# Kernel optimization log

Hardware: AMD Instinct MI355X
Metric: run time of the kernel (lower is better)

The kernel has to match this reference:

```python
import jax, jax.numpy as jnp
import numpy as np

DIM = 384; HEADS = 12; WS = 7; SHIFT = 3
IMG_H = 56; IMG_W = 56; B = 32; MLP_HID = 1536
N = WS * WS; HEAD_DIM = DIM // HEADS


def _rel_pos_index():
    # standard Swin relative position index, shape [N, N], values in [0, (2*WS-1)^2)
    coords = np.stack(np.meshgrid(np.arange(WS), np.arange(WS), indexing='ij')).reshape(2, -1)
    rel = (coords[:, :, None] - coords[:, None, :]).transpose(1, 2, 0)
    rel[..., 0] += WS - 1
    rel[..., 1] += WS - 1
    rel[..., 0] *= 2 * WS - 1
    return jnp.asarray(rel.sum(-1))

REL_IDX = _rel_pos_index()


def _shift_mask():
    # Swin shifted-window attention mask: 0 within region, -100 across regions
    img = np.zeros((IMG_H, IMG_W))
    cnt = 0
    for hs in (slice(0, -WS), slice(-WS, -SHIFT), slice(-SHIFT, None)):
        for ws_ in (slice(0, -WS), slice(-WS, -SHIFT), slice(-SHIFT, None)):
            img[hs, ws_] = cnt
            cnt += 1
    mw = img.reshape(IMG_H // WS, WS, IMG_W // WS, WS).transpose(0, 2, 1, 3).reshape(-1, N)
    am = mw[:, None, :] - mw[:, :, None]
    return jnp.asarray(np.where(am != 0, -100.0, 0.0).astype(np.float32))


def setup_inputs() -> dict:
    key = jax.random.key(0)
    ks = jax.random.split(key, 8)
    rn = lambda k, s: jax.random.normal(k, s, jnp.float32) * 0.02
    return {
        'x': jax.random.normal(ks[0], (B, IMG_H * IMG_W, DIM), jnp.float32),
        'mask': _shift_mask(),
        'w_ln1': jnp.ones((DIM,), jnp.float32), 'b_ln1': jnp.zeros((DIM,), jnp.float32),
        'w_qkv': rn(ks[1], (3 * DIM, DIM)), 'b_qkv': jnp.zeros((3 * DIM,), jnp.float32),
        'rel_bias': rn(ks[2], ((2 * WS - 1) ** 2, HEADS)),
        'w_proj': rn(ks[3], (DIM, DIM)), 'b_proj': jnp.zeros((DIM,), jnp.float32),
        'w_ln2': jnp.ones((DIM,), jnp.float32), 'b_ln2': jnp.zeros((DIM,), jnp.float32),
        'w_fc1': rn(ks[4], (MLP_HID, DIM)), 'b_fc1': jnp.zeros((MLP_HID,), jnp.float32),
        'w_fc2': rn(ks[5], (DIM, MLP_HID)), 'b_fc2': jnp.zeros((DIM,), jnp.float32),
        'H': IMG_H, 'W': IMG_W,
    }


def _ln(x, g, b, eps=1e-5):
    mu = x.mean(-1, keepdims=True)
    var = ((x - mu) ** 2).mean(-1, keepdims=True)
    return (x - mu) * jax.lax.rsqrt(var + eps) * g + b


def reference(x, mask, w_ln1, b_ln1, w_qkv, b_qkv, rel_bias, w_proj, b_proj,
              w_ln2, b_ln2, w_fc1, b_fc1, w_fc2, b_fc2, H, W):
    Bsz, L, C = x.shape
    nW = (H // WS) * (W // WS)
    shortcut = x
    h = _ln(x, w_ln1, b_ln1).reshape(Bsz, H, W, C)
    # cyclic shift
    h = jnp.roll(h, (-SHIFT, -SHIFT), axis=(1, 2))
    # window partition -> [B*nW, N, C]
    h = h.reshape(Bsz, H // WS, WS, W // WS, WS, C).transpose(0, 1, 3, 2, 4, 5).reshape(-1, N, C)
    nB = h.shape[0]
    qkv = (h @ w_qkv.T + b_qkv).reshape(nB, N, 3, HEADS, HEAD_DIM).transpose(2, 0, 3, 1, 4)
    q, k, v = qkv[0] * (HEAD_DIM ** -0.5), qkv[1], qkv[2]  # each [nB, heads, N, hd]
    attn = jnp.einsum('bhnd,bhmd->bhnm', q, k)
    bias = rel_bias[REL_IDX].transpose(2, 0, 1)  # [heads, N, N]
    attn = attn + bias[None]
    attn = attn.reshape(Bsz, nW, HEADS, N, N) + mask[None, :, None]
    attn = jax.nn.softmax(attn, axis=-1).reshape(nB, HEADS, N, N)
    o = jnp.einsum('bhnm,bhmd->bhnd', attn, v).transpose(0, 2, 1, 3).reshape(nB, N, C)
    o = o @ w_proj.T + b_proj
    # window reverse
    o = o.reshape(Bsz, H // WS, W // WS, WS, WS, C).transpose(0, 1, 3, 2, 4, 5).reshape(Bsz, H, W, C)
    o = jnp.roll(o, (SHIFT, SHIFT), axis=(1, 2)).reshape(Bsz, H * W, C)
    x = shortcut + o
    h2 = _ln(x, w_ln2, b_ln2)
    h2 = jax.nn.gelu(h2 @ w_fc1.T + b_fc1) @ w_fc2.T + b_fc2
    return x + h2
```

## Files before the change

### kernel.cpp

```cpp
#include <hip/hip_runtime.h>
#include <stdint.h>

#define B_     32
#define IMG    56
#define L_     (IMG*IMG)
#define C_     384
#define HEADS_ 12
#define HD     32
#define WS_    7
#define N_     49
#define NWIN   64
#define NB     (B_*NWIN)
#define M_TOK  (NB*N_)
#define QKVF   1152

typedef __attribute__((ext_vector_type(8))) short bf16x8;
typedef __attribute__((ext_vector_type(4))) float f32x4;
typedef __attribute__((ext_vector_type(4))) unsigned short u16x4;

__device__ __forceinline__ float bf2f(unsigned short u) {
  union { unsigned int u; float f; } c; c.u = ((unsigned int)u) << 16; return c.f;
}
__device__ __forceinline__ unsigned short f2bf(float f) {
  union { float f; unsigned int u; } c; c.f = f;
  unsigned int r = c.u + 0x7FFFu + ((c.u >> 16) & 1u);
  return (unsigned short)(r >> 16);
}

__device__ __forceinline__ void gload_lds16(const void* g, void* l) {
  __builtin_amdgcn_global_load_lds(
      (const __attribute__((address_space(1))) unsigned int*)(uintptr_t)g,
      (__attribute__((address_space(3))) unsigned int*)(uintptr_t)l,
      16, 0, 0);
}

#define MFMA16(a, b, c) __builtin_amdgcn_mfma_f32_16x16x32_bf16((a), (b), (c), 0, 0, 0)

__global__ __launch_bounds__(256) void k_f2b(const float* __restrict__ src,
                                             ushort* __restrict__ dst, int n) {
  int i = blockIdx.x * 256 + threadIdx.x;
  if (i < n) dst[i] = f2bf(src[i]);
}

template<bool WINDOW>
__global__ __launch_bounds__(256) void k_ln(const float* __restrict__ X,
    const float* __restrict__ G, const float* __restrict__ Bb,
    ushort* __restrict__ out)
{
  int token = blockIdx.x * 4 + (threadIdx.x >> 6);
  int lane  = threadIdx.x & 63;
  const float* xp = X + (size_t)token * C_;
  float v[6];
#pragma unroll
  for (int t = 0; t < 6; t++) v[t] = xp[lane + 64*t];
  float s = 0.f, s2 = 0.f;
#pragma unroll
  for (int t = 0; t < 6; t++) { s += v[t]; s2 += v[t]*v[t]; }
#pragma unroll
  for (int off = 32; off > 0; off >>= 1) {
    s  += __shfl_down(s,  off, 64);
    s2 += __shfl_down(s2, off, 64);
  }
  s = __shfl(s, 0, 64); s2 = __shfl(s2, 0, 64);
  float mu   = s * (1.f / C_);
  float rstd = rsqrtf(s2 * (1.f / C_) - mu * mu + 1e-5f);
  size_t obase;
  if (WINDOW) {
    int b = token / L_, pix = token % L_;
    int hi = pix / IMG, wj = pix % IMG;
    int sh = hi - 3; if (sh < 0) sh += IMG;
    int sw = wj - 3; if (sw < 0) sw += IMG;
    int w = b * NWIN + (sh / WS_) * 8 + (sw / WS_);
    int p = (sh % WS_) * WS_ + (sw % WS_);
    obase = ((size_t)w * N_ + p) * C_;
  } else {
    obase = (size_t)token * C_;
  }
#pragma unroll
  for (int t = 0; t < 6; t++) {
    int c = lane + 64*t;
    out[obase + c] = f2bf((v[t] - mu) * rstd * G[c] + Bb[c]);
  }
}

template<int EPI, typename OutT>
__global__ __launch_bounds__(256, 2) void k_gemm(
    const ushort* __restrict__ A, const ushort* __restrict__ W,
    const float* __restrict__ bias, OutT* __restrict__ out,
    const float* __restrict__ res, int M, int N, int K)
{
  __shared__ __align__(16) ushort As[2][128*32];
  __shared__ __align__(16) ushort Bs[2][128*32];
  int ntn = N >> 7;
  int nwg = gridDim.x;
  int bid = (blockIdx.x & 7) * (nwg >> 3) + (blockIdx.x >> 3);
  int m0 = (bid / ntn) << 7;
  int n0 = (bid % ntn) << 7;
  int tid  = threadIdx.x;
  int wave = tid >> 6, lane = tid & 63;
  int l15  = lane & 15, quad = lane >> 4;
  int wm = (wave & 1) << 6, wn = (wave >> 1) << 6;

  int srow0 = wave * 32 + (lane >> 2);
  int srow1 = srow0 + 16;
  int scol  = (lane & 3) * 8;
  const ushort* gA0 = A + (size_t)(m0 + srow0) * K + scol;
  const ushort* gA1 = A + (size_t)(m0 + srow1) * K + scol;
  const ushort* gB0 = W + (size_t)(n0 + srow0) * K + scol;
  const ushort* gB1 = W + (size_t)(n0 + srow1) * K + scol;
  int oA0 = srow0 * 32 + scol;
  int oA1 = srow1 * 32 + scol;

  f32x4 acc[4][4];
#pragma unroll
  for (int i = 0; i < 4; i++)
#pragma unroll
    for (int j = 0; j < 4; j++) acc[i][j] = (f32x4){0.f, 0.f, 0.f, 0.f};

  gload_lds16(gA0, &As[0][oA0]);
  gload_lds16(gA1, &As[0][oA1]);
  gload_lds16(gB0, &Bs[0][oA0]);
  gload_lds16(gB1, &Bs[0][oA1]);
  gA0 += 32; gA1 += 32; gB0 += 32; gB1 += 32;
  asm volatile("s_waitcnt vmcnt(0)" : : : "memory");
  __syncthreads();

  int nt = K >> 5;
  int cur = 0;
  for (int t = 0; t < nt; t++) {
    int nxt = cur ^ 1;
    if (t + 1 < nt) {
      gload_lds16(gA0, &As[nxt][oA0]);
      gload_lds16(gA1, &As[nxt][oA1]);
      gload_lds16(gB0, &Bs[nxt][oA0]);
      gload_lds16(gB1, &Bs[nxt][oA1]);
      gA0 += 32; gA1 += 32; gB0 += 32; gB1 += 32;
    }
    bf16x8 af[4], bfr[4];
#pragma unroll
    for (int i = 0; i < 4; i++) af[i]  = *(const bf16x8*)&As[cur][(wm + i*16 + l15)*32 + quad*8];
#pragma unroll
    for (int j = 0; j < 4; j++) bfr[j] = *(const bf16x8*)&Bs[cur][(wn + j*16 + l15)*32 + quad*8];
#pragma unroll
    for (int i = 0; i < 4; i++)
#pragma unroll
      for (int j = 0; j < 4; j++)
        acc[i][j] = MFMA16(af[i], bfr[j], acc[i][j]);
    asm volatile("s_waitcnt vmcnt(0)" : : : "memory");
    __syncthreads();
    cur = nxt;
  }

  float bv[4];
#pragma unroll
  for (int j = 0; j < 4; j++) bv[j] = bias[n0 + wn + j*16 + l15];
#pragma unroll
  for (int i = 0; i < 4; i++) {
#pragma unroll
    for (int r = 0; r < 4; r++) {
      int row = m0 + wm + i*16 + quad*4 + r;
      size_t dstbase;
      if (EPI == 1) {
        int w = row / N_, p = row % N_;
        int b = w >> 6, wi = w & 63;
        int hi = (wi >> 3) * WS_ + p / WS_ + 3; if (hi >= IMG) hi -= IMG;
        int wj = (wi & 7)  * WS_ + p % WS_ + 3; if (wj >= IMG) wj -= IMG;
        dstbase = ((size_t)b * L_ + hi * IMG + wj) * C_;
      } else {
        dstbase = (size_t)row * N;
      }
#pragma unroll
      for (int j = 0; j < 4; j++) {
        int col = n0 + wn + j*16 + l15;
        float v = acc[i][j][r] + bv[j];
        if (EPI == 2) {
          v = v / (1.f + __expf(-1.5957691216057308f * (v + 0.044715f * v * v * v)));
        }
        size_t dst = dstbase + col;
        if (EPI == 1) v += res[dst];
        if (EPI == 3) v += res[(size_t)row * N + col];
        if constexpr (sizeof(OutT) == 4) out[dst] = v;
        else                             out[dst] = f2bf(v);
      }
    }
  }
}

__global__ __launch_bounds__(256) void k_bm(const float* __restrict__ relb,
    const float* __restrict__ mask, ushort* __restrict__ bm)
{
  int n = blockIdx.x * 256 + threadIdx.x;
  int r    = n & 3;
  int col  = (n >> 2) & 63;
  int quad = (n >> 8) & 3;
  int i    = (n >> 10) & 3;
  int hw   = n >> 12;
  int h = hw % HEADS_, wc = hw / HEADS_;
  int row = i * 16 + quad * 4 + r;
  float v;
  if (col >= N_) v = -30000.f;
  else if (row >= N_) v = 0.f;
  else {
    int idx = (row / WS_ - col / WS_ + 6) * 13 + (row % WS_ - col % WS_ + 6);
    v = relb[idx * HEADS_ + h] + mask[((size_t)wc * N_ + row) * N_ + col];
  }
  bm[n] = f2bf(v);
}

__global__ __launch_bounds__(256, 3) void k_attn_mfma(
    const ushort* __restrict__ qkv, const ushort* __restrict__ bm,
    ushort* __restrict__ out)
{
  __shared__ __align__(16) ushort Ps[4][64*64];
  __shared__ __align__(16) ushort Vt[4][32*64];
  int wave = threadIdx.x >> 6, lane = threadIdx.x & 63;
  int task = blockIdx.x * 4 + wave;
  int w = task / HEADS_, h = task % HEADS_;
  int l15 = lane & 15, quad = lane >> 4;

  const ushort* base = qkv + (size_t)w * N_ * QKVF + h * HD;

  bf16x8 qf[4], kf[4];
#pragma unroll
  for (int i = 0; i < 4; i++) {
    int rr = i * 16 + l15; if (rr > 48) rr = 48;
    const ushort* rp = base + (size_t)rr * QKVF + quad * 8;
    qf[i] = *(const bf16x8*)rp;
    kf[i] = *(const bf16x8*)(rp + C_);
  }

  {
    int m = lane > 48 ? 48 : lane;
    const ushort* vp = base + (size_t)m * QKVF + 2 * C_;
    bf16x8 v0 = *(const bf16x8*)vp;
    bf16x8 v1 = *(const bf16x8*)(vp + 8);
    bf16x8 v2 = *(const bf16x8*)(vp + 16);
    bf16x8 v3 = *(const bf16x8*)(vp + 24);
    ushort* vt = &Vt[wave][0];
#pragma unroll
    for (int d = 0; d < 32; d++) {
      ushort val = (ushort)(d < 8 ? v0[d & 7] : d < 16 ? v1[d & 7]
                                  : d < 24 ? v2[d & 7] : v3[d & 7]);
      vt[d * 64 + (lane ^ ((d & 7) << 3))] = val;
    }
  }

  f32x4 acc[4][4];
#pragma unroll
  for (int i = 0; i < 4; i++)
#pragma unroll
    for (int j = 0; j < 4; j++) acc[i][j] = (f32x4){0.f, 0.f, 0.f, 0.f};
#pragma unroll
  for (int i = 0; i < 4; i++)
#pragma unroll
    for (int j = 0; j < 4; j++)
      acc[i][j] = MFMA16(qf[i], kf[j], acc[i][j]);

  const ushort* bmb = bm + ((size_t)(w & 63) * HEADS_ + h) * 4096;
  float sv[4][4][4];
#pragma unroll
  for (int i = 0; i < 4; i++)
#pragma unroll
    for (int j = 0; j < 4; j++) {
      u16x4 bv = *(const u16x4*)(bmb + (((i * 4 + quad) * 64) + (j * 16 + l15)) * 4);
#pragma unroll
      for (int r = 0; r < 4; r++)
        sv[i][j][r] = acc[i][j][r] * 0.17677669529663687f + bf2f(bv[r]);
    }

  float mx[4][4], sm[4][4];
#pragma unroll
  for (int i = 0; i < 4; i++)
#pragma unroll
    for (int r = 0; r < 4; r++)
      mx[i][r] = fmaxf(fmaxf(sv[i][0][r], sv[i][1][r]),
                       fmaxf(sv[i][2][r], sv[i][3][r]));
#pragma unroll
  for (int off = 1; off <= 8; off <<= 1)
#pragma unroll
    for (int i = 0; i < 4; i++)
#pragma unroll
      for (int r = 0; r < 4; r++)
        mx[i][r] = fmaxf(mx[i][r], __shfl_xor(mx[i][r], off, 64));
#pragma unroll
  for (int i = 0; i < 4; i++)
#pragma unroll
    for (int r = 0; r < 4; r++) sm[i][r] = 0.f;
#pragma unroll
  for (int i = 0; i < 4; i++)
#pragma unroll
    for (int j = 0; j < 4; j++)
#pragma unroll
      for (int r = 0; r < 4; r++) {
        float e = __expf(sv[i][j][r] - mx[i][r]);
        sv[i][j][r] = e;
        sm[i][r] += e;
      }
#pragma unroll
  for (int off = 1; off <= 8; off <<= 1)
#pragma unroll
    for (int i = 0; i < 4; i++)
#pragma unroll
      for (int r = 0; r < 4; r++)
        sm[i][r] += __shfl_xor(sm[i][r], off, 64);

  ushort* pw = &Ps[wave][0];
#pragma unroll
  for (int i = 0; i < 4; i++)
#pragma unroll
    for (int r = 0; r < 4; r++) {
      float inv = 1.f / sm[i][r];
      int row = i * 16 + quad * 4 + r;
      int s = (row & 7) << 3;
#pragma unroll
      for (int j = 0; j < 4; j++)
        pw[row * 64 + ((j * 16 + l15) ^ s)] = f2bf(sv[i][j][r] * inv);
    }

  f32x4 o[4][2];
#pragma unroll
  for (int i = 0; i < 4; i++)
#pragma unroll
    for (int jv = 0; jv < 2; jv++) o[i][jv] = (f32x4){0.f, 0.f, 0.f, 0.f};
  const ushort* vt = &Vt[wave][0];
#pragma unroll
  for (int ks = 0; ks < 2; ks++) {
    int kc = ks * 32 + quad * 8;
    bf16x8 pa[4], vb[2];
#pragma unroll
    for (int i = 0; i < 4; i++) {
      int row = i * 16 + l15;
      pa[i] = *(const bf16x8*)&pw[row * 64 + (kc ^ ((row & 7) << 3))];
    }
#pragma unroll
    for (int jv = 0; jv < 2; jv++) {
      int nn = jv * 16 + l15;
      vb[jv] = *(const bf16x8*)&vt[nn * 64 + (kc ^ ((nn & 7) << 3))];
    }
#pragma unroll
    for (int i = 0; i < 4; i++)
#pragma unroll
      for (int jv = 0; jv < 2; jv++)
        o[i][jv] = MFMA16(pa[i], vb[jv], o[i][jv]);
  }

  ushort* op = out + ((size_t)w * N_) * C_ + h * HD;
#pragma unroll
  for (int i = 0; i < 4; i++)
#pragma unroll
    for (int r = 0; r < 4; r++) {
      int row = i * 16 + quad * 4 + r;
      if (row < N_) {
#pragma unroll
        for (int jv = 0; jv < 2; jv++)
          op[(size_t)row * C_ + jv * 16 + l15] = f2bf(o[i][jv][r]);
      }
    }
}

extern "C" void kernel_launch(void* const* d_in, const int* in_sizes, int n_in,
                              void* d_out, int out_size, void* d_ws, size_t ws_size,
                              hipStream_t stream) {
  (void)in_sizes; (void)n_in; (void)out_size; (void)ws_size;
  const float* x      = (const float*)d_in[0];
  const float* mask   = (const float*)d_in[1];
  const float* w_ln1  = (const float*)d_in[2];
  const float* b_ln1  = (const float*)d_in[3];
  const float* w_qkv  = (const float*)d_in[4];
  const float* b_qkv  = (const float*)d_in[5];
  const float* relb   = (const float*)d_in[6];
  const float* w_proj = (const float*)d_in[7];
  const float* b_proj = (const float*)d_in[8];
  const float* w_ln2  = (const float*)d_in[9];
  const float* b_ln2  = (const float*)d_in[10];
  const float* w_fc1  = (const float*)d_in[11];
  const float* b_fc1  = (const float*)d_in[12];
  const float* w_fc2  = (const float*)d_in[13];
  const float* b_fc2  = (const float*)d_in[14];

  char* ws = (char*)d_ws;
  ushort* r0 = (ushort*)ws;
  ushort* r1 = (ushort*)(ws + 308281344);
  ushort* bmt = (ushort*)(ws + 231211008);
  ushort* wbq = (ushort*)(ws + 385351680);
  ushort* wbp = wbq + QKVF * C_;
  ushort* wb1 = wbp + C_ * C_;
  ushort* wb2 = wb1 + 1536 * C_;
  float*  x1   = (float*)d_out;
  float*  outp = (float*)d_out;

  k_f2b<<<(QKVF*C_ + 255)/256, 256, 0, stream>>>(w_qkv,  wbq, QKVF*C_);
  k_f2b<<<(C_*C_   + 255)/256, 256, 0, stream>>>(w_proj, wbp, C_*C_);
  k_f2b<<<(1536*C_ + 255)/256, 256, 0, stream>>>(w_fc1,  wb1, 1536*C_);
  k_f2b<<<(C_*1536 + 255)/256, 256, 0, stream>>>(w_fc2,  wb2, C_*1536);
  k_bm<<<(NWIN*HEADS_*4096)/256, 256, 0, stream>>>(relb, mask, bmt);

  k_ln<true ><<<M_TOK/4, 256, 0, stream>>>(x, w_ln1, b_ln1, r1);
  k_gemm<0, ushort><<<(M_TOK/128)*(QKVF/128), 256, 0, stream>>>(
      r1, wbq, b_qkv, r0, nullptr, M_TOK, QKVF, 384);
  k_attn_mfma<<<NB*HEADS_/4, 256, 0, stream>>>(r0, bmt, r1);
  k_gemm<1, float><<<(M_TOK/128)*(C_/128), 256, 0, stream>>>(
      r1, wbp, b_proj, x1, x, M_TOK, C_, 384);
  k_ln<false><<<M_TOK/4, 256, 0, stream>>>(x1, w_ln2, b_ln2, r1);
  k_gemm<2, ushort><<<(M_TOK/128)*(1536/128), 256, 0, stream>>>(
      r1, wb1, b_fc1, r0, nullptr, M_TOK, 1536, 384);
  k_gemm<3, float><<<(M_TOK/128)*(C_/128), 256, 0, stream>>>(
      r0, wb2, b_fc2, outp, x1, M_TOK, C_, 1536);
}
```

Baseline: 1.056 ms.

## Triple-buffer GEMM LDS tiles and XOR-swizzle layout to cut bank conflicts

The GEMM K-loop moves from double to triple buffering of the A and B tiles. Two tiles are prefetched ahead, and the loop waits with vmcnt(4) so the previous stage's global-to-LDS loads can stay in flight, using a single barrier per iteration. The LDS tile layout is also XOR-swizzled: the global source row and chunk are permuted at load time and the fragment reads apply a matching XOR. This is meant to reduce LDS bank conflicts on the 16-byte fragment reads. The cost is 50% more shared memory per block, which may affect the two-blocks-per-CU occupancy target, and more index arithmetic.

```diff
diff --git a/kernel.cpp b/kernel.cpp
--- a/kernel.cpp
+++ b/kernel.cpp
@@ -89,8 +89,8 @@
     const float* __restrict__ bias, OutT* __restrict__ out,
     const float* __restrict__ res, int M, int N, int K)
 {
-  __shared__ __align__(16) ushort As[2][128*32];
-  __shared__ __align__(16) ushort Bs[2][128*32];
+  __shared__ __align__(16) ushort As[3][128*32];
+  __shared__ __align__(16) ushort Bs[3][128*32];
   int ntn = N >> 7;
   int nwg = gridDim.x;
   int bid = (blockIdx.x & 7) * (nwg >> 3) + (blockIdx.x >> 3);
@@ -101,15 +101,17 @@
   int l15  = lane & 15, quad = lane >> 4;
   int wm = (wave & 1) << 6, wn = (wave >> 1) << 6;
 
-  int srow0 = wave * 32 + (lane >> 2);
-  int srow1 = srow0 + 16;
-  int scol  = (lane & 3) * 8;
-  const ushort* gA0 = A + (size_t)(m0 + srow0) * K + scol;
-  const ushort* gA1 = A + (size_t)(m0 + srow1) * K + scol;
-  const ushort* gB0 = W + (size_t)(n0 + srow0) * K + scol;
-  const ushort* gB1 = W + (size_t)(n0 + srow1) * K + scol;
-  int oA0 = srow0 * 32 + scol;
-  int oA1 = srow1 * 32 + scol;
+  int l2 = lane & 3;
+  int R0 = wave * 32 + (lane >> 2);
+  int R1 = R0 + 16;
+  int r0 = R0 ^ ((R0 >> 2) & 1), q0 = l2 ^ (r0 & 3);
+  int r1 = R1 ^ ((R1 >> 2) & 1), q1 = l2 ^ (r1 & 3);
+  const ushort* gA0 = A + (size_t)(m0 + r0) * K + q0 * 8;
+  const ushort* gA1 = A + (size_t)(m0 + r1) * K + q1 * 8;
+  const ushort* gB0 = W + (size_t)(n0 + r0) * K + q0 * 8;
+  const ushort* gB1 = W + (size_t)(n0 + r1) * K + q1 * 8;
+  int o0 = R0 * 32 + l2 * 8;
+  int o1 = R1 * 32 + l2 * 8;
 
   f32x4 acc[4][4];
 #pragma unroll
@@ -117,38 +119,49 @@
 #pragma unroll
     for (int j = 0; j < 4; j++) acc[i][j] = (f32x4){0.f, 0.f, 0.f, 0.f};
 
-  gload_lds16(gA0, &As[0][oA0]);
-  gload_lds16(gA1, &As[0][oA1]);
-  gload_lds16(gB0, &Bs[0][oA0]);
-  gload_lds16(gB1, &Bs[0][oA1]);
+  gload_lds16(gA0, &As[0][o0]);
+  gload_lds16(gA1, &As[0][o1]);
+  gload_lds16(gB0, &Bs[0][o0]);
+  gload_lds16(gB1, &Bs[0][o1]);
   gA0 += 32; gA1 += 32; gB0 += 32; gB1 += 32;
-  asm volatile("s_waitcnt vmcnt(0)" : : : "memory");
-  __syncthreads();
+  gload_lds16(gA0, &As[1][o0]);
+  gload_lds16(gA1, &As[1][o1]);
+  gload_lds16(gB0, &Bs[1][o0]);
+  gload_lds16(gB1, &Bs[1][o1]);
+  gA0 += 32; gA1 += 32; gB0 += 32; gB1 += 32;
 
   int nt = K >> 5;
-  int cur = 0;
+  int cur = 0, stg = 2;
   for (int t = 0; t < nt; t++) {
-    int nxt = cur ^ 1;
-    if (t + 1 < nt) {
-      gload_lds16(gA0, &As[nxt][oA0]);
-      gload_lds16(gA1, &As[nxt][oA1]);
-      gload_lds16(gB0, &Bs[nxt][oA0]);
-      gload_lds16(gB1, &Bs[nxt][oA1]);
+    if (t + 1 < nt) asm volatile("s_waitcnt vmcnt(4)" ::: "memory");
+    else            asm volatile("s_waitcnt vmcnt(0)" ::: "memory");
+    __builtin_amdgcn_s_barrier();
+    asm volatile("" ::: "memory");
+    if (t + 2 < nt) {
+      gload_lds16(gA0, &As[stg][o0]);
+      gload_lds16(gA1, &As[stg][o1]);
+      gload_lds16(gB0, &Bs[stg][o0]);
+      gload_lds16(gB1, &Bs[stg][o1]);
       gA0 += 32; gA1 += 32; gB0 += 32; gB1 += 32;
     }
     bf16x8 af[4], bfr[4];
 #pragma unroll
-    for (int i = 0; i < 4; i++) af[i]  = *(const bf16x8*)&As[cur][(wm + i*16 + l15)*32 + quad*8];
-#pragma unroll
-    for (int j = 0; j < 4; j++) bfr[j] = *(const bf16x8*)&Bs[cur][(wn + j*16 + l15)*32 + quad*8];
+    for (int i = 0; i < 4; i++) {
+      int row = wm + i*16 + l15;
+      af[i]  = *(const bf16x8*)&As[cur][(row*32 + quad*8) ^ ((row & 7) << 3)];
+    }
+#pragma unroll
+    for (int j = 0; j < 4; j++) {
+      int row = wn + j*16 + l15;
+      bfr[j] = *(const bf16x8*)&Bs[cur][(row*32 + quad*8) ^ ((row & 7) << 3)];
+    }
 #pragma unroll
     for (int i = 0; i < 4; i++)
 #pragma unroll
       for (int j = 0; j < 4; j++)
         acc[i][j] = MFMA16(af[i], bfr[j], acc[i][j]);
-    asm volatile("s_waitcnt vmcnt(0)" : : : "memory");
-    __syncthreads();
-    cur = nxt;
+    cur = (cur == 2) ? 0 : cur + 1;
+    stg = (stg == 2) ? 0 : stg + 1;
   }
 
   float bv[4];
```

Measured after the change: 1.062 ms. Within noise of the previous version (+0.6%).
